# Performance work log

Hardware: AMD Instinct MI355X
Metric: run time of the kernel (lower is better)

## Reference

```python
import jax, jax.numpy as jnp
import numpy as np

N_NODES = 50000
N_EDGES = 300000
D = 256
EPS = 1e-12


def setup_inputs() -> dict:
    key = jax.random.key(0)
    ks = jax.random.split(key, 10)
    h5_all = jax.random.normal(ks[0], (N_NODES, D), dtype=jnp.float32)
    edge_index = jax.random.randint(ks[1], (2, N_EDGES), 0, N_NODES, dtype=jnp.int64)
    edge_weight = jax.random.uniform(ks[2], (N_EDGES,), dtype=jnp.float32)
    s = 1.0 / np.sqrt(D)
    W6 = jax.random.normal(ks[3], (D, D), dtype=jnp.float32) * s
    b6 = jnp.zeros((D,), dtype=jnp.float32)
    W7 = jax.random.normal(ks[4], (D, D), dtype=jnp.float32) * s
    b7 = jnp.zeros((D,), dtype=jnp.float32)
    Wp = jax.random.normal(ks[5], (D, D), dtype=jnp.float32) * s
    bp = jnp.zeros((D,), dtype=jnp.float32)
    return {"h5_all": h5_all, "edge_index": edge_index, "edge_weight": edge_weight,
            "W6": W6, "b6": b6, "W7": W7, "b7": b7, "Wp": Wp, "bp": bp}


def _gcn_layer(x, W, b, src, dst, norm, n_nodes):
    # x: [N, D]; transform then gather-scale-scatter along edges
    xt = x @ W                                   # [N, D]
    msg = xt[src] * norm[:, None]                # [E, D] gathered + scaled
    agg = jax.ops.segment_sum(msg, dst, num_segments=n_nodes)  # [N, D]
    return jax.nn.relu(agg + b)


def reference(h5_all, edge_index, edge_weight, W6, b6, W7, b7, Wp, bp):
    src, dst = edge_index[0], edge_index[1]
    # symmetric degree normalization with edge weights (GCN-style)
    deg_out = jax.ops.segment_sum(edge_weight, src, num_segments=N_NODES)
    deg_in = jax.ops.segment_sum(edge_weight, dst, num_segments=N_NODES)
    norm = edge_weight * jax.lax.rsqrt(deg_out[src] * deg_in[dst] + EPS)  # [E]
    h6 = _gcn_layer(h5_all, W6, b6, src, dst, norm, N_NODES)
    h7 = _gcn_layer(h6, W7, b7, src, dst, norm, N_NODES)
    out = h7 @ Wp + bp                           # post_mp linear head
    return out
```

## Files before the change

### kernel.cpp

```cpp
#include <hip/hip_runtime.h>

#define N_NODES 50000
#define N_PAD   50048
#define N_PANELS 3125
#define N_EDGES 300000
#define EPS_F 1e-12f
#define EB ((N_EDGES + 255) / 256)
#define GB 512
#define SCAN_NB ((N_NODES + 255) / 256)
#define MASK48 ((1ull << 48) - 1)
#define ZBYTES (N_NODES * 20)

typedef _Float16 f16x8 __attribute__((ext_vector_type(8)));
typedef float f32x4 __attribute__((ext_vector_type(4)));

static __device__ inline f32x4 mfma_f16(f16x8 a, f16x8 b, f32x4 c) {
    return __builtin_amdgcn_mfma_f32_16x16x32_f16(a, b, c, 0, 0, 0);
}

static __device__ inline size_t swz(int row, int l) {
    return ((size_t)(row >> 4) * 8 + (l >> 2)) * 512 + (size_t)((l & 3) * 128 + (row & 15) * 8);
}


__global__ __launch_bounds__(256) void zero_kernel(int4* __restrict__ p, int n16) {
    int i = blockIdx.x * 256 + threadIdx.x;
    if (i < n16) p[i] = make_int4(0, 0, 0, 0);
}


__global__ __launch_bounds__(256) void p1_kernel(const int* __restrict__ ei,
                                                 const float* __restrict__ ew,
                                                 unsigned long long* __restrict__ pk_out,
                                                 unsigned long long* __restrict__ pk_in,
                                                 const float* __restrict__ W6,
                                                 const float* __restrict__ W7,
                                                 const float* __restrict__ Wp,
                                                 _Float16* __restrict__ Bsw) {
    int b = blockIdx.x;
    if (b < EB) {
        int e = b * 256 + threadIdx.x;
        if (e >= N_EDGES) return;
        int s = ei[e];
        int d = ei[N_EDGES + e];
        unsigned long long wfx = (unsigned long long)(ew[e] * 4294967296.0f);
        atomicAdd(&pk_out[s], wfx);
        atomicAdd(&pk_in[d], (1ull << 48) | wfx);
    } else {
        int bb = b - EB;
        int wsel = bb >> 5;
        const float* W = (wsel == 0) ? W6 : (wsel == 1) ? W7 : Wp;
        int id = (bb & 31) * 256 + threadIdx.x;
        int n = id >> 5, l = id & 31;
        f16x8 o;
#pragma unroll
        for (int j = 0; j < 8; ++j)
            o[j] = (_Float16)W[(l * 8 + j) * 256 + n];
        *(f16x8*)&Bsw[(size_t)wsel * 65536 + swz(n, l)] = o;
    }
}


__global__ __launch_bounds__(256) void scan1_kernel(const unsigned long long* __restrict__ pk_in,
                                                    const unsigned long long* __restrict__ pk_out,
                                                    float* __restrict__ deg_in,
                                                    float* __restrict__ deg_out,
                                                    int* __restrict__ partial) {
    __shared__ int sh[256];
    int i = blockIdx.x * 256 + threadIdx.x;
    int c = 0;
    if (i < N_NODES) {
        unsigned long long p = pk_in[i];
        c = (int)(p >> 48);
        deg_in[i] = (float)(p & MASK48) * 0x1p-32f;
        deg_out[i] = (float)pk_out[i] * 0x1p-32f;
    }
    sh[threadIdx.x] = c;
    __syncthreads();
    for (int off = 128; off > 0; off >>= 1) {
        if (threadIdx.x < (unsigned)off) sh[threadIdx.x] += sh[threadIdx.x + off];
        __syncthreads();
    }
    if (threadIdx.x == 0) partial[blockIdx.x] = sh[0];
}

__global__ __launch_bounds__(256) void scan23_kernel(const unsigned long long* __restrict__ pk_in,
                                                     const int* __restrict__ partial,
                                                     int* __restrict__ row_ptr) {
    __shared__ int ps[256];
    __shared__ int sh[256];
    int t = threadIdx.x;
    int pv = (t < SCAN_NB) ? partial[t] : 0;
    ps[t] = pv;
    __syncthreads();
    for (int off = 1; off < 256; off <<= 1) {
        int x = (t >= off) ? ps[t - off] : 0;
        __syncthreads();
        ps[t] += x;
        __syncthreads();
    }
    int incl = ps[t];
    __syncthreads();
    ps[t] = incl - pv;
    __syncthreads();
    const int boff = ps[blockIdx.x];

    int i = blockIdx.x * 256 + t;
    int v = (i < N_NODES) ? (int)(pk_in[i] >> 48) : 0;
    sh[t] = v;
    __syncthreads();
    for (int off = 1; off < 256; off <<= 1) {
        int x = (t >= off) ? sh[t - off] : 0;
        __syncthreads();
        sh[t] += x;
        __syncthreads();
    }
    if (i < N_NODES) row_ptr[i] = sh[t] - v + boff;
    if (i == 0) row_ptr[N_NODES] = N_EDGES;
}


__global__ __launch_bounds__(256) void p2_kernel(const int* __restrict__ ei,
                                                 const float* __restrict__ ew,
                                                 const float* __restrict__ deg_out,
                                                 const float* __restrict__ deg_in,
                                                 const int* __restrict__ row_ptr,
                                                 int* __restrict__ cur,
                                                 int2* __restrict__ csr,
                                                 const float* __restrict__ h5,
                                                 const _Float16* __restrict__ Bsw,
                                                 _Float16* __restrict__ xt) {
    __shared__ _Float16 ebuf[4][16 * 72];

    if (blockIdx.x < EB) {
        int e = blockIdx.x * 256 + threadIdx.x;
        if (e >= N_EDGES) return;
        int s = ei[e];
        int d = ei[N_EDGES + e];
        float nm = ew[e] * rsqrtf(deg_out[s] * deg_in[d] + EPS_F);
        int pos = atomicAdd(&cur[d], 1);
        csr[row_ptr[d] + pos] = make_int2(s, __float_as_int(nm));
        return;
    }

    const int t = threadIdx.x;
    const int w = t >> 6, lane = t & 63;

    f16x8 bf[4][8];
#pragma unroll
    for (int cp4 = 0; cp4 < 4; ++cp4)
#pragma unroll
        for (int kb = 0; kb < 8; ++kb)
            bf[cp4][kb] = *(const f16x8*)&Bsw[(size_t)((w * 4 + cp4) * 8 + kb) * 512 + lane * 8];

    for (int p = blockIdx.x - EB; p < N_PANELS; p += GB) {
        const float* ab = &h5[(size_t)(p * 16 + (lane & 15)) * 256 + (lane >> 4) * 8];
        f16x8 af[8];
#pragma unroll
        for (int kb = 0; kb < 8; ++kb) {
            float4 v0 = *(const float4*)(ab + kb * 32);
            float4 v1 = *(const float4*)(ab + kb * 32 + 4);
            f16x8 a;
            a[0] = (_Float16)v0.x; a[1] = (_Float16)v0.y;
            a[2] = (_Float16)v0.z; a[3] = (_Float16)v0.w;
            a[4] = (_Float16)v1.x; a[5] = (_Float16)v1.y;
            a[6] = (_Float16)v1.z; a[7] = (_Float16)v1.w;
            af[kb] = a;
        }

        f32x4 acc[4];
#pragma unroll
        for (int cp4 = 0; cp4 < 4; ++cp4) acc[cp4] = (f32x4){0.f, 0.f, 0.f, 0.f};
#pragma unroll
        for (int kb = 0; kb < 8; ++kb)
#pragma unroll
            for (int cp4 = 0; cp4 < 4; ++cp4)
                acc[cp4] = mfma_f16(af[kb], bf[cp4][kb], acc[cp4]);

        _Float16* eb = ebuf[w];
        const int rq = 4 * (lane >> 4);
        const int lr = lane & 15;
#pragma unroll
        for (int cp4 = 0; cp4 < 4; ++cp4)
#pragma unroll
            for (int rr = 0; rr < 4; ++rr)
                eb[(rq + rr) * 72 + cp4 * 16 + lr] = (_Float16)acc[cp4][rr];
#pragma unroll
        for (int it = 0; it < 2; ++it) {
            int rl = it * 8 + (lane >> 3);
            f16x8 v = *(const f16x8*)&eb[rl * 72 + (lane & 7) * 8];
            *(f16x8*)&xt[(size_t)(p * 16 + rl) * 256 + w * 64 + (lane & 7) * 8] = v;
        }
    }
}


template <int MODE>
__global__ __launch_bounds__(256) void gemm_f16(const _Float16* __restrict__ Asw,
                                                const _Float16* __restrict__ Bsw,
                                                const float* __restrict__ bias,
                                                void* __restrict__ Cout) {
    __shared__ _Float16 ebuf[4][16 * 72];

    const int t = threadIdx.x;
    const int w = t >> 6, lane = t & 63;
    const int lr = lane & 15;

    f16x8 bf[4][8];
#pragma unroll
    for (int cp4 = 0; cp4 < 4; ++cp4)
#pragma unroll
        for (int kb = 0; kb < 8; ++kb)
            bf[cp4][kb] = *(const f16x8*)&Bsw[(size_t)((w * 4 + cp4) * 8 + kb) * 512 + lane * 8];

    float bc[4];
    if (MODE == 1) {
#pragma unroll
        for (int cp4 = 0; cp4 < 4; ++cp4) bc[cp4] = bias[w * 64 + cp4 * 16 + lr];
    }

    for (int p = blockIdx.x; p < N_PANELS; p += GB) {
        const _Float16* abase = &Asw[(size_t)p * 4096 + lane * 8];
        f16x8 af[8];
#pragma unroll
        for (int kb = 0; kb < 8; ++kb)
            af[kb] = *(const f16x8*)&abase[kb * 512];

        f32x4 acc[4];
#pragma unroll
        for (int cp4 = 0; cp4 < 4; ++cp4) acc[cp4] = (f32x4){0.f, 0.f, 0.f, 0.f};
#pragma unroll
        for (int kb = 0; kb < 8; ++kb)
#pragma unroll
            for (int cp4 = 0; cp4 < 4; ++cp4)
                acc[cp4] = mfma_f16(af[kb], bf[cp4][kb], acc[cp4]);

        if (MODE == 0) {
            _Float16* eb = ebuf[w];
            const int rq = 4 * (lane >> 4);
#pragma unroll
            for (int cp4 = 0; cp4 < 4; ++cp4)
#pragma unroll
                for (int rr = 0; rr < 4; ++rr)
                    eb[(rq + rr) * 72 + cp4 * 16 + lr] = (_Float16)acc[cp4][rr];
            _Float16* xp = (_Float16*)Cout;
#pragma unroll
            for (int it = 0; it < 2; ++it) {
                int rl = it * 8 + (lane >> 3);
                f16x8 v = *(const f16x8*)&eb[rl * 72 + (lane & 7) * 8];
                *(f16x8*)&xp[(size_t)(p * 16 + rl) * 256 + w * 64 + (lane & 7) * 8] = v;
            }
        } else {
            float* op = (float*)Cout;
            const int rbase = p * 16 + 4 * (lane >> 4);
#pragma unroll
            for (int cp4 = 0; cp4 < 4; ++cp4) {
                const int col = w * 64 + cp4 * 16 + lr;
#pragma unroll
                for (int rr = 0; rr < 4; ++rr)
                    op[(size_t)(rbase + rr) * 256 + col] = acc[cp4][rr] + bc[cp4];
            }
        }
    }
}


__global__ __launch_bounds__(256) void agg_kernel(const _Float16* __restrict__ xt,
                                                  const int* __restrict__ row_ptr,
                                                  const int2* __restrict__ csr,
                                                  const float* __restrict__ bias,
                                                  _Float16* __restrict__ Asw) {
    const int g = threadIdx.x >> 5;
    const int l = threadIdx.x & 31;
    const int v = blockIdx.x * 8 + g;
    const int d0 = l * 8;

    const int s0 = row_ptr[v];
    const int s1 = row_ptr[v + 1];

    float acc[8] = {0.f, 0.f, 0.f, 0.f, 0.f, 0.f, 0.f, 0.f};

    int i = s0;
    for (; i + 4 <= s1; i += 4) {
        int2 hd[4];
#pragma unroll
        for (int u = 0; u < 4; ++u) hd[u] = csr[i + u];
        f16x8 val[4];
#pragma unroll
        for (int u = 0; u < 4; ++u)
            val[u] = *(const f16x8*)&xt[(size_t)hd[u].x * 256 + d0];
#pragma unroll
        for (int u = 0; u < 4; ++u) {
            float wv = __int_as_float(hd[u].y);
#pragma unroll
            for (int j = 0; j < 8; ++j)
                acc[j] += (float)val[u][j] * wv;
        }
    }
    {
        int rem = s1 - i;
        int2 hd[3];
#pragma unroll
        for (int u = 0; u < 3; ++u)
            hd[u] = (u < rem) ? csr[i + u] : make_int2(0, 0);
        f16x8 val[3];
#pragma unroll
        for (int u = 0; u < 3; ++u)
            val[u] = *(const f16x8*)&xt[(size_t)hd[u].x * 256 + d0];
#pragma unroll
        for (int u = 0; u < 3; ++u) {
            float wv = __int_as_float(hd[u].y);
#pragma unroll
            for (int j = 0; j < 8; ++j)
                acc[j] += (float)val[u][j] * wv;
        }
    }

    f16x8 o;
#pragma unroll
    for (int j = 0; j < 8; ++j) {
        float r = acc[j] + bias[d0 + j];
        r = r > 0.f ? r : 0.f;
        o[j] = (_Float16)r;
    }
    *(f16x8*)&Asw[swz(v, l)] = o;
}


extern "C" void kernel_launch(void* const* d_in, const int* in_sizes, int n_in,
                              void* d_out, int out_size, void* d_ws, size_t ws_size,
                              hipStream_t stream) {
    (void)in_sizes; (void)n_in; (void)out_size; (void)ws_size;
    const float* h5 = (const float*)d_in[0];
    const int*   ei = (const int*)d_in[1];
    const float* ew = (const float*)d_in[2];
    const float* W6 = (const float*)d_in[3];
    const float* b6 = (const float*)d_in[4];
    const float* W7 = (const float*)d_in[5];
    const float* b7 = (const float*)d_in[6];
    const float* Wp = (const float*)d_in[7];
    const float* bp = (const float*)d_in[8];
    float* out = (float*)d_out;

    char* ws = (char*)d_ws;
    size_t off = 0;
    auto alloc = [&](size_t bytes) -> void* {
        void* p = ws + off;
        off = (off + bytes + 255) & ~(size_t)255;
        return p;
    };

    char* zblk = (char*)alloc(ZBYTES);
    unsigned long long* pk_out = (unsigned long long*)zblk;
    unsigned long long* pk_in  = (unsigned long long*)(zblk + N_NODES * 8);
    int* cur = (int*)(zblk + N_NODES * 16);

    float* deg_out = (float*)alloc(N_NODES * 4);
    float* deg_in  = (float*)alloc(N_NODES * 4);
    int*   row_ptr = (int*)alloc((N_NODES + 1) * 4);
    int*   partial = (int*)alloc(SCAN_NB * 4);
    int2*  csr     = (int2*)alloc(N_EDGES * 8);
    _Float16* Bsw  = (_Float16*)alloc(3 * 65536 * 2);
    _Float16* Asw  = (_Float16*)alloc((size_t)N_PAD * 256 * 2);
    _Float16* xt   = (_Float16*)alloc((size_t)N_PAD * 256 * 2);

    const int Z16 = ZBYTES / 16;

    zero_kernel<<<(Z16 + 255) / 256, 256, 0, stream>>>((int4*)zblk, Z16);

    p1_kernel<<<EB + 96, 256, 0, stream>>>(ei, ew, pk_out, pk_in, W6, W7, Wp, Bsw);
    scan1_kernel<<<SCAN_NB, 256, 0, stream>>>(pk_in, pk_out, deg_in, deg_out, partial);
    scan23_kernel<<<SCAN_NB, 256, 0, stream>>>(pk_in, partial, row_ptr);

    p2_kernel<<<EB + GB, 256, 0, stream>>>(ei, ew, deg_out, deg_in, row_ptr, cur, csr,
                                           h5, Bsw, xt);

    agg_kernel<<<N_NODES / 8, 256, 0, stream>>>(xt, row_ptr, csr, b6, Asw);
    gemm_f16<0><<<GB, 256, 0, stream>>>(Asw, Bsw + 65536, nullptr, xt);
    agg_kernel<<<N_NODES / 8, 256, 0, stream>>>(xt, row_ptr, csr, b7, Asw);
    gemm_f16<1><<<GB, 256, 0, stream>>>(Asw, Bsw + 2 * 65536, bp, out);
}
```

Before: 170.9 us.

## Split fused edge-fill/GEMM kernel, widen grids, stage fp32 output, unroll aggregation by 8

The fused p2 kernel is split into a standalone edge-fill kernel and an h5 GEMM kernel, which is launched right after the weight preparation and before the scans. The GEMM grids grow from 512 to 1024 blocks. The final fp32 GEMM now stages its results through shared memory so it can write coalesced float4 rows, and the aggregation loop is unrolled to 8 edges with a 7-wide tail. These changes target store coalescing, memory-level parallelism in the gathers, and occupancy, at the cost of an extra kernel launch and higher register pressure.

```diff
diff --git a/kernel.cpp b/kernel.cpp
--- a/kernel.cpp
+++ b/kernel.cpp
@@ -1,12 +1,11 @@
 #include <hip/hip_runtime.h>
 
 #define N_NODES 50000
-#define N_PAD   50048
 #define N_PANELS 3125
 #define N_EDGES 300000
 #define EPS_F 1e-12f
 #define EB ((N_EDGES + 255) / 256)
-#define GB 512
+#define GRID 1024
 #define SCAN_NB ((N_NODES + 255) / 256)
 #define MASK48 ((1ull << 48) - 1)
 #define ZBYTES (N_NODES * 20)
@@ -119,29 +118,24 @@
     if (i == 0) row_ptr[N_NODES] = N_EDGES;
 }
 
-
-__global__ __launch_bounds__(256) void p2_kernel(const int* __restrict__ ei,
-                                                 const float* __restrict__ ew,
-                                                 const float* __restrict__ deg_out,
-                                                 const float* __restrict__ deg_in,
-                                                 const int* __restrict__ row_ptr,
-                                                 int* __restrict__ cur,
-                                                 int2* __restrict__ csr,
-                                                 const float* __restrict__ h5,
-                                                 const _Float16* __restrict__ Bsw,
-                                                 _Float16* __restrict__ xt) {
-    __shared__ _Float16 ebuf[4][16 * 72];
-
-    if (blockIdx.x < EB) {
-        int e = blockIdx.x * 256 + threadIdx.x;
-        if (e >= N_EDGES) return;
-        int s = ei[e];
-        int d = ei[N_EDGES + e];
-        float nm = ew[e] * rsqrtf(deg_out[s] * deg_in[d] + EPS_F);
-        int pos = atomicAdd(&cur[d], 1);
-        csr[row_ptr[d] + pos] = make_int2(s, __float_as_int(nm));
-        return;
-    }
+__global__ void fill_kernel(const int* __restrict__ ei, const float* __restrict__ ew,
+                            const float* __restrict__ deg_out, const float* __restrict__ deg_in,
+                            const int* __restrict__ row_ptr, int* __restrict__ cur,
+                            int2* __restrict__ csr) {
+    int e = blockIdx.x * blockDim.x + threadIdx.x;
+    if (e >= N_EDGES) return;
+    int s = ei[e];
+    int d = ei[N_EDGES + e];
+    float nm = ew[e] * rsqrtf(deg_out[s] * deg_in[d] + EPS_F);
+    int pos = atomicAdd(&cur[d], 1);
+    csr[row_ptr[d] + pos] = make_int2(s, __float_as_int(nm));
+}
+
+
+__global__ __launch_bounds__(256) void gemm_h5(const float* __restrict__ h5,
+                                               const _Float16* __restrict__ Bsw,
+                                               _Float16* __restrict__ xt) {
+    __shared__ __align__(16) _Float16 ebuf[4][16 * 72];
 
     const int t = threadIdx.x;
     const int w = t >> 6, lane = t & 63;
@@ -153,7 +147,7 @@
         for (int kb = 0; kb < 8; ++kb)
             bf[cp4][kb] = *(const f16x8*)&Bsw[(size_t)((w * 4 + cp4) * 8 + kb) * 512 + lane * 8];
 
-    for (int p = blockIdx.x - EB; p < N_PANELS; p += GB) {
+    for (int p = blockIdx.x; p < N_PANELS; p += GRID) {
         const float* ab = &h5[(size_t)(p * 16 + (lane & 15)) * 256 + (lane >> 4) * 8];
         f16x8 af[8];
 #pragma unroll
@@ -200,7 +194,7 @@
                                                 const _Float16* __restrict__ Bsw,
                                                 const float* __restrict__ bias,
                                                 void* __restrict__ Cout) {
-    __shared__ _Float16 ebuf[4][16 * 72];
+    __shared__ __align__(16) char ebraw[4][16 * 68 * 4];
 
     const int t = threadIdx.x;
     const int w = t >> 6, lane = t & 63;
@@ -219,7 +213,7 @@
         for (int cp4 = 0; cp4 < 4; ++cp4) bc[cp4] = bias[w * 64 + cp4 * 16 + lr];
     }
 
-    for (int p = blockIdx.x; p < N_PANELS; p += GB) {
+    for (int p = blockIdx.x; p < N_PANELS; p += GRID) {
         const _Float16* abase = &Asw[(size_t)p * 4096 + lane * 8];
         f16x8 af[8];
 #pragma unroll
@@ -235,9 +229,9 @@
             for (int cp4 = 0; cp4 < 4; ++cp4)
                 acc[cp4] = mfma_f16(af[kb], bf[cp4][kb], acc[cp4]);
 
+        const int rq = 4 * (lane >> 4);
         if (MODE == 0) {
-            _Float16* eb = ebuf[w];
-            const int rq = 4 * (lane >> 4);
+            _Float16* eb = (_Float16*)ebraw[w];
 #pragma unroll
             for (int cp4 = 0; cp4 < 4; ++cp4)
 #pragma unroll
@@ -251,14 +245,18 @@
                 *(f16x8*)&xp[(size_t)(p * 16 + rl) * 256 + w * 64 + (lane & 7) * 8] = v;
             }
         } else {
+            float* eb = (float*)ebraw[w];
+#pragma unroll
+            for (int cp4 = 0; cp4 < 4; ++cp4)
+#pragma unroll
+                for (int rr = 0; rr < 4; ++rr)
+                    eb[(rq + rr) * 68 + cp4 * 16 + lr] = acc[cp4][rr] + bc[cp4];
             float* op = (float*)Cout;
-            const int rbase = p * 16 + 4 * (lane >> 4);
-#pragma unroll
-            for (int cp4 = 0; cp4 < 4; ++cp4) {
-                const int col = w * 64 + cp4 * 16 + lr;
-#pragma unroll
-                for (int rr = 0; rr < 4; ++rr)
-                    op[(size_t)(rbase + rr) * 256 + col] = acc[cp4][rr] + bc[cp4];
+#pragma unroll
+            for (int it = 0; it < 4; ++it) {
+                int rl = it * 4 + (lane >> 4);
+                float4 v = *(const float4*)&eb[rl * 68 + lr * 4];
+                *(float4*)&op[(size_t)(p * 16 + rl) * 256 + w * 64 + lr * 4] = v;
             }
         }
     }
@@ -281,34 +279,34 @@
     float acc[8] = {0.f, 0.f, 0.f, 0.f, 0.f, 0.f, 0.f, 0.f};
 
     int i = s0;
-    for (; i + 4 <= s1; i += 4) {
-        int2 hd[4];
-#pragma unroll
-        for (int u = 0; u < 4; ++u) hd[u] = csr[i + u];
-        f16x8 val[4];
-#pragma unroll
-        for (int u = 0; u < 4; ++u)
+    for (; i + 8 <= s1; i += 8) {
+        int2 hd[8];
+#pragma unroll
+        for (int u = 0; u < 8; ++u) hd[u] = csr[i + u];
+        f16x8 val[8];
+#pragma unroll
+        for (int u = 0; u < 8; ++u)
             val[u] = *(const f16x8*)&xt[(size_t)hd[u].x * 256 + d0];
 #pragma unroll
-        for (int u = 0; u < 4; ++u) {
+        for (int u = 0; u < 8; ++u) {
             float wv = __int_as_float(hd[u].y);
 #pragma unroll
             for (int j = 0; j < 8; ++j)
                 acc[j] += (float)val[u][j] * wv;
         }
     }
-    {
-        int rem = s1 - i;
-        int2 hd[3];
-#pragma unroll
-        for (int u = 0; u < 3; ++u)
+    int rem = s1 - i;
+    if (rem) {
+        int2 hd[7];
+#pragma unroll
+        for (int u = 0; u < 7; ++u)
             hd[u] = (u < rem) ? csr[i + u] : make_int2(0, 0);
-        f16x8 val[3];
-#pragma unroll
-        for (int u = 0; u < 3; ++u)
+        f16x8 val[7];
+#pragma unroll
+        for (int u = 0; u < 7; ++u)
             val[u] = *(const f16x8*)&xt[(size_t)hd[u].x * 256 + d0];
 #pragma unroll
-        for (int u = 0; u < 3; ++u) {
+        for (int u = 0; u < 7; ++u) {
             float wv = __int_as_float(hd[u].y);
 #pragma unroll
             for (int j = 0; j < 8; ++j)
@@ -361,22 +359,23 @@
     int*   partial = (int*)alloc(SCAN_NB * 4);
     int2*  csr     = (int2*)alloc(N_EDGES * 8);
     _Float16* Bsw  = (_Float16*)alloc(3 * 65536 * 2);
-    _Float16* Asw  = (_Float16*)alloc((size_t)N_PAD * 256 * 2);
-    _Float16* xt   = (_Float16*)alloc((size_t)N_PAD * 256 * 2);
+    _Float16* Asw  = (_Float16*)alloc((size_t)N_NODES * 256 * 2);
+    _Float16* xt   = (_Float16*)alloc((size_t)N_NODES * 256 * 2);
 
     const int Z16 = ZBYTES / 16;
 
     zero_kernel<<<(Z16 + 255) / 256, 256, 0, stream>>>((int4*)zblk, Z16);
 
     p1_kernel<<<EB + 96, 256, 0, stream>>>(ei, ew, pk_out, pk_in, W6, W7, Wp, Bsw);
+
+    gemm_h5<<<GRID, 256, 0, stream>>>(h5, Bsw, xt);
+
     scan1_kernel<<<SCAN_NB, 256, 0, stream>>>(pk_in, pk_out, deg_in, deg_out, partial);
     scan23_kernel<<<SCAN_NB, 256, 0, stream>>>(pk_in, partial, row_ptr);
-
-    p2_kernel<<<EB + GB, 256, 0, stream>>>(ei, ew, deg_out, deg_in, row_ptr, cur, csr,
-                                           h5, Bsw, xt);
+    fill_kernel<<<EB, 256, 0, stream>>>(ei, ew, deg_out, deg_in, row_ptr, cur, csr);
 
     agg_kernel<<<N_NODES / 8, 256, 0, stream>>>(xt, row_ptr, csr, b6, Asw);
-    gemm_f16<0><<<GB, 256, 0, stream>>>(Asw, Bsw + 65536, nullptr, xt);
+    gemm_f16<0><<<GRID, 256, 0, stream>>>(Asw, Bsw + 65536, nullptr, xt);
     agg_kernel<<<N_NODES / 8, 256, 0, stream>>>(xt, row_ptr, csr, b7, Asw);
-    gemm_f16<1><<<GB, 256, 0, stream>>>(Asw, Bsw + 2 * 65536, bp, out);
-}
+    gemm_f16<1><<<GRID, 256, 0, stream>>>(Asw, Bsw + 2 * 65536, bp, out);
+}
```

Result: slower. 191.3 us (+11.9%).
